# Optimization experiments

Measured on AMD Instinct MI355X. Metric: run time of the kernel, lower is better.

## Reference

```python
import jax, jax.numpy as jnp
import numpy as np

ORDER = 4


def setup_inputs() -> dict:
    key = jax.random.key(0)
    k1, k2, k3, k4 = jax.random.split(key, 4)
    B, IN, OUT = 8192, 1024, 1024
    x = jax.random.normal(k1, (B, IN), dtype=jnp.float32)
    base_weight = jax.random.normal(k2, (OUT, IN), dtype=jnp.float32) * (1.0 / np.sqrt(IN))
    std = 1.0 / (IN * np.sqrt(ORDER))
    taylor_coeffs = jax.random.normal(k3, (OUT, IN, ORDER), dtype=jnp.float32) * std
    bound = 1.0 / np.sqrt(IN)
    bias = jax.random.uniform(k4, (OUT,), dtype=jnp.float32, minval=-bound, maxval=bound)
    return {"x": x, "base_weight": base_weight, "taylor_coeffs": taylor_coeffs, "bias": bias}


def reference(x, base_weight, taylor_coeffs, bias):
    # base path: SiLU(x) @ W^T
    base_out = jnp.einsum('bi,oi->bo', jax.nn.silu(x), base_weight)
    # taylor path: x_powers[b,i,k] = x**k, k=0..ORDER-1; contract with coeffs[o,i,k]
    powers = jnp.arange(ORDER, dtype=x.dtype)  # [K]
    x_powers = x[:, :, None] ** powers  # [B, IN, K]
    taylor_out = jnp.einsum('bik,oik->bo', x_powers, taylor_coeffs)
    return base_out + taylor_out + bias
```

## Files before the change

### kernel.cpp

```cpp
#include <hip/hip_runtime.h>
#include <hip/hip_bf16.h>

#define GLOBAL_AS __attribute__((address_space(1)))
#define LDS_AS    __attribute__((address_space(3)))

typedef __bf16 bf16x8 __attribute__((ext_vector_type(8)));
typedef float  f32x4  __attribute__((ext_vector_type(4)));

constexpr int BATCH = 8192;
constexpr int IN    = 1024;
constexpr int OUT   = 1024;
constexpr int KDIM  = IN * 4;
constexpr int TM = 128, TN = 128, BK = 64;
constexpr int NKT = KDIM / BK;

__device__ __forceinline__ unsigned short f2bf(float f) {
    union { float f; unsigned u; } v; v.f = f;
    unsigned r = v.u + 0x7fffu + ((v.u >> 16) & 1u);
    return (unsigned short)(r >> 16);
}
__device__ __forceinline__ unsigned pk(unsigned short a, unsigned short b) {
    return (unsigned)a | ((unsigned)b << 16);
}

__global__ __launch_bounds__(256) void prep(const float* __restrict__ x,
                                            const float* __restrict__ W,
                                            const float* __restrict__ C,
                                            const float* __restrict__ bias,
                                            unsigned short* __restrict__ Ab,
                                            unsigned short* __restrict__ Bb,
                                            float* __restrict__ be) {
    if (blockIdx.x < 8192) {
        int idx = blockIdx.x * 256 + threadIdx.x;
        float4 v = reinterpret_cast<const float4*>(x)[idx];
        float e0[4] = {v.x, v.y, v.z, v.w};
        unsigned short o[16];
#pragma unroll
        for (int j = 0; j < 4; ++j) {
            float xv = e0[j];
            float s  = xv / (1.0f + __expf(-xv));
            float x2 = xv * xv;
            o[4*j+0] = f2bf(s);
            o[4*j+1] = f2bf(xv);
            o[4*j+2] = f2bf(x2);
            o[4*j+3] = f2bf(x2 * xv);
        }
        uint4 d0 = make_uint4(pk(o[0],o[1]), pk(o[2],o[3]),   pk(o[4],o[5]),   pk(o[6],o[7]));
        uint4 d1 = make_uint4(pk(o[8],o[9]), pk(o[10],o[11]), pk(o[12],o[13]), pk(o[14],o[15]));
        uint4* dst = reinterpret_cast<uint4*>(Ab) + (size_t)idx * 2;
        dst[0] = d0;
        dst[1] = d1;
    } else {
        const int o = blockIdx.x - 8192, t = threadIdx.x;
        const int i0 = t * 4;
        const float4* c4 = reinterpret_cast<const float4*>(C + ((size_t)o * IN + i0) * 4);
        float4 w4 = *reinterpret_cast<const float4*>(W + (size_t)o * IN + i0);
        float wv[4] = {w4.x, w4.y, w4.z, w4.w};
        float s = 0.f;
        unsigned d[8];
#pragma unroll
        for (int j = 0; j < 4; ++j) {
            float4 c = c4[j];
            s += c.x;
            d[2*j]   = pk(f2bf(wv[j]), f2bf(c.y));
            d[2*j+1] = pk(f2bf(c.z),   f2bf(c.w));
        }
        uint4* dst = reinterpret_cast<uint4*>(Bb + (size_t)o * KDIM + i0 * 4);
        dst[0] = make_uint4(d[0], d[1], d[2], d[3]);
        dst[1] = make_uint4(d[4], d[5], d[6], d[7]);
#pragma unroll
        for (int off = 32; off > 0; off >>= 1) s += __shfl_down(s, off, 64);
        __shared__ float red[4];
        if ((t & 63) == 0) red[t >> 6] = s;
        __syncthreads();
        if (t == 0) be[o] = bias[o] + red[0] + red[1] + red[2] + red[3];
    }
}

__global__ __launch_bounds__(256, 2) void gemm_kan(
        const unsigned short* __restrict__ Ab,
        const unsigned short* __restrict__ Bb,
        const float* __restrict__ be,
        float* __restrict__ out) {
    __shared__ unsigned short sA[2][TM * BK];
    __shared__ unsigned short sB[2][TN * BK];

    const int t   = threadIdx.x;
    const int l   = blockIdx.x;
    const int bm  = (l & 7) * 8 + ((l >> 3) & 7);
    const int bn  = l >> 6;
    const int lane = t & 63;
    const int wave = t >> 6;
    const int wr   = wave >> 1;
    const int wc   = wave & 1;
    const int l15  = lane & 15;
    const int quad = lane >> 4;

    const int rowT = t >> 3;
    const int gT   = (t & 7) ^ (rowT & 7);
    const unsigned short* pa[4];
    const unsigned short* pb[4];
#pragma unroll
    for (int i = 0; i < 4; ++i) {
        pa[i] = Ab + (size_t)(bm * TM + i * 32 + rowT) * KDIM + gT * 8;
        pb[i] = Bb + (size_t)(bn * TN + i * 32 + rowT) * KDIM + gT * 8;
    }

    f32x4 acc[4][4];
    const f32x4 zero = {0.f, 0.f, 0.f, 0.f};
#pragma unroll
    for (int i = 0; i < 4; ++i)
#pragma unroll
        for (int j = 0; j < 4; ++j) acc[i][j] = zero;

    const int xr = l15 & 7;

#pragma unroll
    for (int i = 0; i < 4; ++i) {
        __builtin_amdgcn_global_load_lds((const GLOBAL_AS void*)pa[i],
                                         (LDS_AS void*)(sA[0] + i * 2048 + t * 8), 16, 0, 0);
        __builtin_amdgcn_global_load_lds((const GLOBAL_AS void*)pb[i],
                                         (LDS_AS void*)(sB[0] + i * 2048 + t * 8), 16, 0, 0);
    }

    for (int kt = 0; kt < NKT; ++kt) {
        __syncthreads();

        if (kt + 1 < NKT) {
            const int koff = (kt + 1) * BK;
            const int nb = (kt + 1) & 1;
#pragma unroll
            for (int i = 0; i < 4; ++i) {
                __builtin_amdgcn_global_load_lds((const GLOBAL_AS void*)(pa[i] + koff),
                                                 (LDS_AS void*)(sA[nb] + i * 2048 + t * 8), 16, 0, 0);
                __builtin_amdgcn_global_load_lds((const GLOBAL_AS void*)(pb[i] + koff),
                                                 (LDS_AS void*)(sB[nb] + i * 2048 + t * 8), 16, 0, 0);
            }
        }

        const unsigned short* a_base = sA[kt & 1];
        const unsigned short* b_base = sB[kt & 1];
#pragma unroll
        for (int kk = 0; kk < 2; ++kk) {
            const int cq = ((kk * 4 + quad) ^ xr) * 8;
            bf16x8 af[4], bv[4];
#pragma unroll
            for (int mi = 0; mi < 4; ++mi)
                af[mi] = *reinterpret_cast<const bf16x8*>(
                    a_base + (wr * 64 + mi * 16 + l15) * BK + cq);
#pragma unroll
            for (int ni = 0; ni < 4; ++ni)
                bv[ni] = *reinterpret_cast<const bf16x8*>(
                    b_base + (wc * 64 + ni * 16 + l15) * BK + cq);
#pragma unroll
            for (int mi = 0; mi < 4; ++mi)
#pragma unroll
                for (int ni = 0; ni < 4; ++ni)
                    acc[mi][ni] = __builtin_amdgcn_mfma_f32_16x16x32_bf16(
                        af[mi], bv[ni], acc[mi][ni], 0, 0, 0);
        }
    }

    float bev[4];
#pragma unroll
    for (int ni = 0; ni < 4; ++ni)
        bev[ni] = be[bn * TN + wc * 64 + ni * 16 + l15];

#pragma unroll
    for (int mi = 0; mi < 4; ++mi) {
        const int grow = bm * TM + wr * 64 + mi * 16 + quad * 4;
#pragma unroll
        for (int ni = 0; ni < 4; ++ni) {
            const int gcol = bn * TN + wc * 64 + ni * 16 + l15;
            float* po = out + (size_t)grow * OUT + gcol;
#pragma unroll
            for (int r = 0; r < 4; ++r)
                po[(size_t)r * OUT] = acc[mi][ni][r] + bev[ni];
        }
    }
}

extern "C" void kernel_launch(void* const* d_in, const int* in_sizes, int n_in,
                              void* d_out, int out_size, void* d_ws, size_t ws_size,
                              hipStream_t stream) {
    const float* x    = (const float*)d_in[0];
    const float* W    = (const float*)d_in[1];
    const float* C    = (const float*)d_in[2];
    const float* bias = (const float*)d_in[3];
    float* out = (float*)d_out;

    unsigned short* Ab = (unsigned short*)d_ws;
    unsigned short* Bb = Ab + (size_t)BATCH * KDIM;
    float*          be = (float*)(Bb + (size_t)OUT * KDIM);

    prep<<<dim3(8192 + 1024), dim3(256), 0, stream>>>(x, W, C, bias, Ab, Bb, be);

    gemm_kan<<<dim3(512), dim3(256), 0, stream>>>(Ab, Bb, be, out);
}
```

Before: 176.4 us.

## Restructure GEMM into 128x256 tiles with 8 waves and triple-buffered LDS pipeline

Switches the bf16 GEMM from 128x128 tiles with 4 waves and double buffering to 128x256 tiles with 8 waves and a three-stage LDS ring. Global-to-LDS copies run two tiles ahead, split into halves that interleave with MFMA phases, with explicit waitcnt/barrier control and setprio around the MFMA blocks. Block-to-tile mapping is also changed to group tiles by XCD. This aims to raise data reuse per block and hide load latency, at the cost of more LDS per block (144KB) and many more barriers per iteration, which can limit occupancy and add sync overhead.

```diff
diff --git a/kernel.cpp b/kernel.cpp
--- a/kernel.cpp
+++ b/kernel.cpp
@@ -11,8 +11,9 @@
 constexpr int IN    = 1024;
 constexpr int OUT   = 1024;
 constexpr int KDIM  = IN * 4;
-constexpr int TM = 128, TN = 128, BK = 64;
-constexpr int NKT = KDIM / BK;
+constexpr int BM = 128, BN = 256, BK = 64;
+constexpr int NKT  = KDIM / BK;
+constexpr int LDSBUF = 24576;
 
 __device__ __forceinline__ unsigned short f2bf(float f) {
     union { float f; unsigned u; } v; v.f = f;
@@ -77,34 +78,35 @@
     }
 }
 
-__global__ __launch_bounds__(256, 2) void gemm_kan(
+__global__ __launch_bounds__(512, 2) void gemm_kan(
         const unsigned short* __restrict__ Ab,
         const unsigned short* __restrict__ Bb,
         const float* __restrict__ be,
         float* __restrict__ out) {
-    __shared__ unsigned short sA[2][TM * BK];
-    __shared__ unsigned short sB[2][TN * BK];
-
-    const int t   = threadIdx.x;
-    const int l   = blockIdx.x;
-    const int bm  = (l & 7) * 8 + ((l >> 3) & 7);
-    const int bn  = l >> 6;
+    extern __shared__ unsigned short smem[];
+
+    const int t    = threadIdx.x;
+    const int l    = blockIdx.x;
+    const int xcd  = l & 7;
+    const int bn   = xcd >> 1;
+    const int bm   = (xcd & 1) * 32 + (l >> 3);
     const int lane = t & 63;
     const int wave = t >> 6;
-    const int wr   = wave >> 1;
-    const int wc   = wave & 1;
+    const int wr   = wave >> 2;
+    const int wc   = wave & 3;
     const int l15  = lane & 15;
     const int quad = lane >> 4;
+    const int x7   = l15 & 7;
 
     const int rowT = t >> 3;
-    const int gT   = (t & 7) ^ (rowT & 7);
-    const unsigned short* pa[4];
-    const unsigned short* pb[4];
-#pragma unroll
-    for (int i = 0; i < 4; ++i) {
-        pa[i] = Ab + (size_t)(bm * TM + i * 32 + rowT) * KDIM + gT * 8;
-        pb[i] = Bb + (size_t)(bn * TN + i * 32 + rowT) * KDIM + gT * 8;
-    }
+    const int chT  = (t & 7) ^ (rowT & 7);
+    const unsigned short* aS = Ab + (size_t)(bm * BM + rowT) * KDIM + chT * 8;
+    const unsigned short* bS = Bb + (size_t)(bn * BN + rowT) * KDIM + chT * 8;
+
+    const int aRd = (wr * 32 + l15) * 64;
+    const int bRd = 8192 + (wc * 64 + l15) * 64;
+    const int ck0 = (quad ^ x7) * 8;
+    const int ck1 = ((4 + quad) ^ x7) * 8;
 
     f32x4 acc[4][4];
     const f32x4 zero = {0.f, 0.f, 0.f, 0.f};
@@ -113,69 +115,105 @@
 #pragma unroll
         for (int j = 0; j < 4; ++j) acc[i][j] = zero;
 
-    const int xr = l15 & 7;
-
-#pragma unroll
-    for (int i = 0; i < 4; ++i) {
-        __builtin_amdgcn_global_load_lds((const GLOBAL_AS void*)pa[i],
-                                         (LDS_AS void*)(sA[0] + i * 2048 + t * 8), 16, 0, 0);
-        __builtin_amdgcn_global_load_lds((const GLOBAL_AS void*)pb[i],
-                                         (LDS_AS void*)(sB[0] + i * 2048 + t * 8), 16, 0, 0);
-    }
-
+#define STAGE_A(tile, buf, h)                                                          \
+    __builtin_amdgcn_global_load_lds(                                                  \
+        (const GLOBAL_AS void*)(aS + (size_t)(tile) * BK + (size_t)(h) * 64 * KDIM),   \
+        (LDS_AS void*)(smem + (buf) * LDSBUF + (h) * 4096 + t * 8), 16, 0, 0)
+
+#define STAGE_B(tile, buf, h) do {                                                     \
+    const unsigned short* s_ = bS + (size_t)(tile) * BK + (size_t)(h) * 128 * KDIM;    \
+    unsigned short* d_ = smem + (buf) * LDSBUF + 8192 + (h) * 8192 + t * 8;            \
+    __builtin_amdgcn_global_load_lds((const GLOBAL_AS void*)s_, (LDS_AS void*)d_,      \
+                                     16, 0, 0);                                        \
+    __builtin_amdgcn_global_load_lds((const GLOBAL_AS void*)(s_ + (size_t)64 * KDIM),  \
+                                     (LDS_AS void*)(d_ + 4096), 16, 0, 0);             \
+} while (0)
+
+    STAGE_A(0, 0, 0); STAGE_B(0, 0, 0); STAGE_A(0, 0, 1); STAGE_B(0, 0, 1);
+    STAGE_A(1, 1, 0); STAGE_B(1, 1, 0); STAGE_A(1, 1, 1); STAGE_B(1, 1, 1);
+    asm volatile("s_waitcnt vmcnt(6)" ::: "memory");
+    __builtin_amdgcn_s_barrier();
+
+    int cb = 0;
     for (int kt = 0; kt < NKT; ++kt) {
-        __syncthreads();
-
-        if (kt + 1 < NKT) {
-            const int koff = (kt + 1) * BK;
-            const int nb = (kt + 1) & 1;
-#pragma unroll
-            for (int i = 0; i < 4; ++i) {
-                __builtin_amdgcn_global_load_lds((const GLOBAL_AS void*)(pa[i] + koff),
-                                                 (LDS_AS void*)(sA[nb] + i * 2048 + t * 8), 16, 0, 0);
-                __builtin_amdgcn_global_load_lds((const GLOBAL_AS void*)(pb[i] + koff),
-                                                 (LDS_AS void*)(sB[nb] + i * 2048 + t * 8), 16, 0, 0);
-            }
-        }
-
-        const unsigned short* a_base = sA[kt & 1];
-        const unsigned short* b_base = sB[kt & 1];
-#pragma unroll
-        for (int kk = 0; kk < 2; ++kk) {
-            const int cq = ((kk * 4 + quad) ^ xr) * 8;
-            bf16x8 af[4], bv[4];
-#pragma unroll
-            for (int mi = 0; mi < 4; ++mi)
-                af[mi] = *reinterpret_cast<const bf16x8*>(
-                    a_base + (wr * 64 + mi * 16 + l15) * BK + cq);
-#pragma unroll
-            for (int ni = 0; ni < 4; ++ni)
-                bv[ni] = *reinterpret_cast<const bf16x8*>(
-                    b_base + (wc * 64 + ni * 16 + l15) * BK + cq);
-#pragma unroll
-            for (int mi = 0; mi < 4; ++mi)
+        const unsigned short* sb = smem + cb * LDSBUF;
+        const int  nb = (cb >= 1) ? cb - 1 : 2;
+        const bool pf = (kt + 2) < NKT;
+
+        bf16x8 av[2][2], bvv[4][2];
+
+        av[0][0] = *reinterpret_cast<const bf16x8*>(sb + aRd + ck0);
+        av[0][1] = *reinterpret_cast<const bf16x8*>(sb + aRd + ck1);
+        av[1][0] = *reinterpret_cast<const bf16x8*>(sb + aRd + 1024 + ck0);
+        av[1][1] = *reinterpret_cast<const bf16x8*>(sb + aRd + 1024 + ck1);
+#pragma unroll
+        for (int ni = 0; ni < 4; ++ni) {
+            bvv[ni][0] = *reinterpret_cast<const bf16x8*>(sb + bRd + ni * 1024 + ck0);
+            bvv[ni][1] = *reinterpret_cast<const bf16x8*>(sb + bRd + ni * 1024 + ck1);
+        }
+        if (pf) { STAGE_A(kt + 2, nb, 0); STAGE_B(kt + 2, nb, 0); }
+        __builtin_amdgcn_s_barrier();
+        asm volatile("s_waitcnt lgkmcnt(0)" ::: "memory");
+        __builtin_amdgcn_sched_barrier(0);
+        __builtin_amdgcn_s_setprio(1);
+#pragma unroll
+        for (int kk = 0; kk < 2; ++kk)
+#pragma unroll
+            for (int mi = 0; mi < 2; ++mi)
 #pragma unroll
                 for (int ni = 0; ni < 4; ++ni)
                     acc[mi][ni] = __builtin_amdgcn_mfma_f32_16x16x32_bf16(
-                        af[mi], bv[ni], acc[mi][ni], 0, 0, 0);
-        }
-    }
+                        av[mi][kk], bvv[ni][kk], acc[mi][ni], 0, 0, 0);
+        __builtin_amdgcn_s_setprio(0);
+        __builtin_amdgcn_s_barrier();
+
+        av[0][0] = *reinterpret_cast<const bf16x8*>(sb + aRd + 4096 + ck0);
+        av[0][1] = *reinterpret_cast<const bf16x8*>(sb + aRd + 4096 + ck1);
+        av[1][0] = *reinterpret_cast<const bf16x8*>(sb + aRd + 5120 + ck0);
+        av[1][1] = *reinterpret_cast<const bf16x8*>(sb + aRd + 5120 + ck1);
+        if (pf) { STAGE_A(kt + 2, nb, 1); STAGE_B(kt + 2, nb, 1); }
+        __builtin_amdgcn_s_barrier();
+        asm volatile("s_waitcnt lgkmcnt(0)" ::: "memory");
+        __builtin_amdgcn_sched_barrier(0);
+        __builtin_amdgcn_s_setprio(1);
+#pragma unroll
+        for (int kk = 0; kk < 2; ++kk)
+#pragma unroll
+            for (int mi = 0; mi < 2; ++mi)
+#pragma unroll
+                for (int ni = 0; ni < 4; ++ni)
+                    acc[2 + mi][ni] = __builtin_amdgcn_mfma_f32_16x16x32_bf16(
+                        av[mi][kk], bvv[ni][kk], acc[2 + mi][ni], 0, 0, 0);
+        __builtin_amdgcn_s_setprio(0);
+
+        if (kt < NKT - 2) {
+            asm volatile("s_waitcnt vmcnt(6)" ::: "memory");
+            __builtin_amdgcn_s_barrier();
+        } else if (kt == NKT - 2) {
+            asm volatile("s_waitcnt vmcnt(0)" ::: "memory");
+            __builtin_amdgcn_s_barrier();
+        }
+        cb = (cb == 2) ? 0 : cb + 1;
+    }
+
+#undef STAGE_A
+#undef STAGE_B
 
     float bev[4];
 #pragma unroll
     for (int ni = 0; ni < 4; ++ni)
-        bev[ni] = be[bn * TN + wc * 64 + ni * 16 + l15];
-
-#pragma unroll
-    for (int mi = 0; mi < 4; ++mi) {
-        const int grow = bm * TM + wr * 64 + mi * 16 + quad * 4;
+        bev[ni] = be[bn * BN + wc * 64 + ni * 16 + l15];
+
+#pragma unroll
+    for (int mg = 0; mg < 4; ++mg) {
+        const int grow = bm * BM + (mg >> 1) * 64 + wr * 32 + (mg & 1) * 16 + quad * 4;
 #pragma unroll
         for (int ni = 0; ni < 4; ++ni) {
-            const int gcol = bn * TN + wc * 64 + ni * 16 + l15;
+            const int gcol = bn * BN + wc * 64 + ni * 16 + l15;
             float* po = out + (size_t)grow * OUT + gcol;
 #pragma unroll
             for (int r = 0; r < 4; ++r)
-                po[(size_t)r * OUT] = acc[mi][ni][r] + bev[ni];
+                po[(size_t)r * OUT] = acc[mg][ni][r] + bev[ni];
         }
     }
 }
@@ -193,7 +231,15 @@
     unsigned short* Bb = Ab + (size_t)BATCH * KDIM;
     float*          be = (float*)(Bb + (size_t)OUT * KDIM);
 
+    constexpr int LDS_BYTES = 3 * LDSBUF * 2;
+    static bool inited = false;
+    if (!inited) {
+        hipFuncSetAttribute(reinterpret_cast<const void*>(&gemm_kan),
+                            hipFuncAttributeMaxDynamicSharedMemorySize, LDS_BYTES);
+        inited = true;
+    }
+
     prep<<<dim3(8192 + 1024), dim3(256), 0, stream>>>(x, W, C, bias, Ab, Bb, be);
 
-    gemm_kan<<<dim3(512), dim3(256), 0, stream>>>(Ab, Bb, be, out);
-}
+    gemm_kan<<<dim3(256), dim3(512), LDS_BYTES, stream>>>(Ab, Bb, be, out);
+}
```

After: 176.9 us. No clear change (+0.3%).
